# Kernel tuning notes

Measured on AMD Instinct MI355X. Metric: run time of the kernel, lower is better.

The kernel has to match this reference:

```python
import jax, jax.numpy as jnp
import numpy as np


def setup_inputs() -> dict:
    key = jax.random.key(0)
    k1, k2, k3, k4 = jax.random.split(key, 4)
    B, H, S, D = 2, 16, 2048, 64
    q = jax.random.normal(k1, (B, H, S, D), dtype=jnp.float32)
    k = jax.random.normal(k2, (B, H, S, D), dtype=jnp.float32)
    v = jax.random.normal(k3, (B, H, S, D), dtype=jnp.float32)
    mask = jax.random.randint(k4, (1, 1, S, S), 0, 2, dtype=jnp.int32)
    return {"q": q, "k": k, "v": v, "mask": mask}


def reference(q, k, v, mask):
    # scores: [B,H,S,S] -- intentionally materialized as in the original
    d = k.shape[-1]
    scale = 1.0 / jnp.sqrt(jnp.asarray(d, dtype=q.dtype))
    x = jnp.einsum("bhqd,bhkd->bhqk", q, k) * scale
    x = x + mask.astype(x.dtype) * jnp.asarray(-10000.0, dtype=x.dtype)
    p = jax.nn.softmax(x, axis=-1)  # dropout is identity in eval mode
    return jnp.einsum("bhqk,bhkd->bhqd", p, v)
```

## Files before the change

### kernel.cpp

```cpp
#include <hip/hip_runtime.h>


#define S_LEN 2048
#define D_DIM 64
#define N_KT 32
#define LDK 72
#define LDV 72
#define TILE_SHORTS (64 * 72)
#define TILE_BYTES (TILE_SHORTS * 2)
#define NBH 32

typedef __attribute__((ext_vector_type(8))) short bf16x8;
typedef __attribute__((ext_vector_type(16))) float f32x16;
typedef __attribute__((ext_vector_type(2))) __fp16 fp16x2;
typedef unsigned int u32;
typedef unsigned long long u64;

#define C1 0.180336880111121f
#define CM (-14426.9504088896f)

static __device__ __forceinline__ unsigned short f2bf(float f) {
  union { float f; unsigned u; } x; x.f = f;
  return (unsigned short)((x.u + 0x8000u) >> 16);
}
static __device__ __forceinline__ unsigned packbf(float lo, float hi) {
  union { float f; unsigned u; } a, b; a.f = lo; b.f = hi;
  return ((a.u + 0x8000u) >> 16) | ((b.u + 0x8000u) & 0xffff0000u);
}
static __device__ __forceinline__ f32x16 zero16() {
  f32x16 z;
#pragma unroll
  for (int i = 0; i < 16; ++i) z[i] = 0.f;
  return z;
}
static __device__ __forceinline__ void dma16(const u32* g, u32* l) {
  __builtin_amdgcn_global_load_lds(
      (const __attribute__((address_space(1))) u32*)g,
      (__attribute__((address_space(3))) u32*)l, 16, 0, 0);
}
static __device__ __forceinline__ unsigned pkh(float lo, float hi) {
  union { fp16x2 h; unsigned u; } x;
  x.h = __builtin_amdgcn_cvt_pkrtz(lo, hi);
  return x.u;
}

__global__ __launch_bounds__(256) void prep_kv(
    const float* __restrict__ k, const float* __restrict__ v,
    unsigned short* __restrict__ kws, unsigned short* __restrict__ vws) {
  const int kt = blockIdx.x, bh = blockIdx.y;
  const int t = threadIdx.x;
  __shared__ unsigned short Vt[TILE_SHORTS];
  const size_t goff = (size_t)bh * (S_LEN * D_DIM) + (size_t)kt * 64 * D_DIM;
  const float4* kg = (const float4*)(k + goff);
  const float4* vg = (const float4*)(v + goff);
  unsigned short* kimg = kws + (size_t)(bh * N_KT + kt) * TILE_SHORTS;
#pragma unroll
  for (int j = 0; j < 4; ++j) {
    const int i = t + j * 256;
    const int row = i >> 4, c4 = i & 15;
    const float4 x = kg[i];
    ushort4 w;
    w.x = f2bf(x.x); w.y = f2bf(x.y); w.z = f2bf(x.z); w.w = f2bf(x.w);
    *(ushort4*)&kimg[row * LDK + c4 * 4] = w;
    const float4 y = vg[i];
    const int swc = 8 * (((row >> 3) + c4) & 7) + (row & 7);
    const unsigned p01 = pkh(y.x, y.y);
    const unsigned p23 = pkh(y.z, y.w);
    Vt[(4 * c4 + 0) * LDV + swc] = (unsigned short)(p01 & 0xffff);
    Vt[(4 * c4 + 1) * LDV + swc] = (unsigned short)(p01 >> 16);
    Vt[(4 * c4 + 2) * LDV + swc] = (unsigned short)(p23 & 0xffff);
    Vt[(4 * c4 + 3) * LDV + swc] = (unsigned short)(p23 >> 16);
  }
  __syncthreads();
  uint4* vimg = (uint4*)(vws + (size_t)(bh * N_KT + kt) * TILE_SHORTS);
  const uint4* lv = (const uint4*)Vt;
  for (int i = t; i < TILE_BYTES / 16; i += 256) vimg[i] = lv[i];
}

__global__ __launch_bounds__(256) void prep_mask(
    const int* __restrict__ mask, u32* __restrict__ mw) {
  const int wid = blockIdx.x * 4 + (threadIdx.x >> 6);
  const int lane = threadIdx.x & 63;
  const int row = wid >> 5, kt = wid & 31;
  const int mv = mask[(size_t)row * S_LEN + kt * 64 + lane];
  const u64 b = __ballot(mv != 0);
  if (lane < 32) {
    const int hl = lane >> 4, p = lane & 15;
    const int kb = p >> 3, g = (p >> 1) & 3, h = p & 1;
    const int j0 = 32 * kb + 8 * g + 4 * hl + 2 * h;
    u32 w = 0;
    if (!((b >> j0) & 1)) w |= 0x0000FFFFu;
    if (!((b >> (j0 + 1)) & 1)) w |= 0xFFFF0000u;
    mw[((size_t)(row * 2 + hl) * N_KT + kt) * 16 + p] = w;
  }
}

__global__ __launch_bounds__(128, 2) void attn_fwd(
    const float* __restrict__ q, const unsigned short* __restrict__ kws,
    const unsigned short* __restrict__ vws, const u32* __restrict__ mw,
    float* __restrict__ out) {
  const int qt = blockIdx.x;
  const int bh = blockIdx.y;
  const size_t hoff = (size_t)bh * (S_LEN * D_DIM);

  __shared__ unsigned short Ks[2][TILE_SHORTS];
  __shared__ unsigned short Vt[2][TILE_SHORTS];

  const int t = threadIdx.x;
  const int wave = t >> 6;
  const int lane = t & 63;
  const int col = lane & 31;
  const int hl = lane >> 5;
  const int sw = col >> 2;

  const int qg = qt * 64 + wave * 32 + col;

  bf16x8 bQ[4];
  {
    const float* qrow = q + hoff + (size_t)qg * D_DIM;
#pragma unroll
    for (int ks = 0; ks < 4; ++ks) {
      const float4 x0 = *(const float4*)(qrow + ks * 16 + hl * 8);
      const float4 x1 = *(const float4*)(qrow + ks * 16 + hl * 8 + 4);
      union { bf16x8 v; unsigned d[4]; } u;
      u.d[0] = packbf(x0.x * C1, x0.y * C1);
      u.d[1] = packbf(x0.z * C1, x0.w * C1);
      u.d[2] = packbf(x1.x * C1, x1.y * C1);
      u.d[3] = packbf(x1.z * C1, x1.w * C1);
      bQ[ks] = u.v;
    }
  }

  bf16x8 onesA;
  {
    union { bf16x8 v; unsigned d[4]; } u;
    u.d[0] = u.d[1] = u.d[2] = u.d[3] = 0x3C003C00u;
    onesA = u.v;
  }

  const unsigned short* kbase = kws + (size_t)bh * N_KT * TILE_SHORTS;
  const unsigned short* vbase = vws + (size_t)bh * N_KT * TILE_SHORTS;

  f32x16 oT0 = zero16(), oT1 = zero16(), oL = zero16();
  const uint4* mrow = (const uint4*)(mw + (size_t)(qg * 2 + hl) * N_KT * 16);

  {
    const u32* g = (const u32*)((wave == 0 ? kbase : vbase));
    u32* l = wave == 0 ? (u32*)&Ks[0][0] : (u32*)&Vt[0][0];
#pragma unroll
    for (int i = 0; i < 9; ++i) dma16(g + i * 256 + lane * 4, l + i * 256);
  }

  for (int kt = 0; kt < N_KT; ++kt) {
    __syncthreads();
    if (kt + 1 < N_KT) {
      const u32* g = (const u32*)((wave == 0 ? kbase : vbase) +
                                  (size_t)(kt + 1) * TILE_SHORTS);
      u32* l = wave == 0 ? (u32*)&Ks[(kt + 1) & 1][0]
                         : (u32*)&Vt[(kt + 1) & 1][0];
#pragma unroll
      for (int i = 0; i < 9; ++i) dma16(g + i * 256 + lane * 4, l + i * 256);
    }
    uint4 mq0 = mrow[kt * 4 + 0], mq1 = mrow[kt * 4 + 1];
    uint4 mq2 = mrow[kt * 4 + 2], mq3 = mrow[kt * 4 + 3];
    const u32 mwv[16] = {mq0.x, mq0.y, mq0.z, mq0.w, mq1.x, mq1.y, mq1.z, mq1.w,
                         mq2.x, mq2.y, mq2.z, mq2.w, mq3.x, mq3.y, mq3.z, mq3.w};
    const unsigned short* Ksb = Ks[kt & 1];
    const unsigned short* Vtb = Vt[kt & 1];

    f32x16 sT0 = zero16(), sT1 = zero16();
#pragma unroll
    for (int ks = 0; ks < 4; ++ks) {
      const bf16x8 aK0 = *(const bf16x8*)&Ksb[col * LDK + ks * 16 + hl * 8];
      const bf16x8 aK1 = *(const bf16x8*)&Ksb[(32 + col) * LDK + ks * 16 + hl * 8];
      sT0 = __builtin_amdgcn_mfma_f32_32x32x16_bf16(aK0, bQ[ks], sT0, 0, 0, 0);
      sT1 = __builtin_amdgcn_mfma_f32_32x32x16_bf16(aK1, bQ[ks], sT1, 0, 0, 0);
    }

    unsigned pw[16];
#pragma unroll
    for (int kb = 0; kb < 2; ++kb) {
      const f32x16 sT = kb ? sT1 : sT0;
#pragma unroll
      for (int g = 0; g < 4; ++g) {
        const float e0 = __builtin_amdgcn_exp2f(sT[g * 4 + 0]);
        const float e1 = __builtin_amdgcn_exp2f(sT[g * 4 + 1]);
        const float e2 = __builtin_amdgcn_exp2f(sT[g * 4 + 2]);
        const float e3 = __builtin_amdgcn_exp2f(sT[g * 4 + 3]);
        pw[kb * 8 + g * 2 + 0] = pkh(e0, e1) & mwv[kb * 8 + g * 2 + 0];
        pw[kb * 8 + g * 2 + 1] = pkh(e2, e3) & mwv[kb * 8 + g * 2 + 1];
      }
    }

#pragma unroll
    for (int ks = 0; ks < 4; ++ks) {
      const int kb = ks >> 1, h = ks & 1;
      const unsigned d0 = pw[kb * 8 + 4 * h + 0], d1 = pw[kb * 8 + 4 * h + 1];
      const unsigned d2 = pw[kb * 8 + 4 * h + 2], d3 = pw[kb * 8 + 4 * h + 3];
      const unsigned s0 = hl ? d0 : d2;
      const unsigned s1 = hl ? d1 : d3;
      const unsigned r0 = (unsigned)__shfl_xor((int)s0, 32);
      const unsigned r1 = (unsigned)__shfl_xor((int)s1, 32);
      union { bf16x8 v; unsigned d[4]; } pf;
      pf.d[0] = hl ? r0 : d0;
      pf.d[1] = hl ? r1 : d1;
      pf.d[2] = hl ? d2 : r0;
      pf.d[3] = hl ? d3 : r1;
      const int cpr = 8 * (((2 * ks + hl) + sw) & 7);
      const bf16x8 aV0 = *(const bf16x8*)&Vtb[col * LDV + cpr];
      const bf16x8 aV1 = *(const bf16x8*)&Vtb[(32 + col) * LDV + cpr];
      oT0 = __builtin_amdgcn_mfma_f32_32x32x16_f16(aV0, pf.v, oT0, 0, 0, 0);
      oT1 = __builtin_amdgcn_mfma_f32_32x32x16_f16(aV1, pf.v, oT1, 0, 0, 0);
      oL = __builtin_amdgcn_mfma_f32_32x32x16_f16(onesA, pf.v, oL, 0, 0, 0);
    }
  }

  const float inv = 1.0f / oL[0];
  float* orow = out + hoff + (size_t)qg * D_DIM;
#pragma unroll
  for (int rg = 0; rg < 4; ++rg) {
    float4 w0, w1;
    w0.x = oT0[rg * 4 + 0] * inv; w0.y = oT0[rg * 4 + 1] * inv;
    w0.z = oT0[rg * 4 + 2] * inv; w0.w = oT0[rg * 4 + 3] * inv;
    w1.x = oT1[rg * 4 + 0] * inv; w1.y = oT1[rg * 4 + 1] * inv;
    w1.z = oT1[rg * 4 + 2] * inv; w1.w = oT1[rg * 4 + 3] * inv;
    *(float4*)(orow + 8 * rg + 4 * hl) = w0;
    *(float4*)(orow + 32 + 8 * rg + 4 * hl) = w1;
  }
}

__global__ __launch_bounds__(256, 2) void attn_fwd_self(
    const float* __restrict__ q, const float* __restrict__ k,
    const float* __restrict__ v, const int* __restrict__ mask,
    float* __restrict__ out) {
  const int qt = blockIdx.x;
  const int bh = blockIdx.y;
  const size_t hoff = (size_t)bh * (S_LEN * D_DIM);
  __shared__ unsigned short Ks[64 * LDK];
  __shared__ unsigned short Vt[64 * LDV];
  const int t = threadIdx.x;
  const int wave = t >> 6;
  const int lane = t & 63;
  const int col = lane & 31;
  const int hl = lane >> 5;
  const int sw = col >> 2;
  const int qg = qt * 128 + wave * 32 + col;
  bf16x8 bQ[4];
  {
    const float* qrow = q + hoff + (size_t)qg * D_DIM;
#pragma unroll
    for (int ks = 0; ks < 4; ++ks) {
      const float4 x0 = *(const float4*)(qrow + ks * 16 + hl * 8);
      const float4 x1 = *(const float4*)(qrow + ks * 16 + hl * 8 + 4);
      union { bf16x8 v; unsigned d[4]; } u;
      u.d[0] = packbf(x0.x, x0.y);
      u.d[1] = packbf(x0.z, x0.w);
      u.d[2] = packbf(x1.x, x1.y);
      u.d[3] = packbf(x1.z, x1.w);
      bQ[ks] = u.v;
    }
  }
  float4 pk[4], pv[4];
  {
    const float4* kg = (const float4*)(k + hoff);
    const float4* vg = (const float4*)(v + hoff);
#pragma unroll
    for (int j = 0; j < 4; ++j) { pk[j] = kg[t + j * 256]; pv[j] = vg[t + j * 256]; }
  }
  f32x16 oT0 = zero16(), oT1 = zero16();
  float lacc = 0.f;
  const int* mrow = mask + (size_t)qg * S_LEN;
  for (int kt = 0; kt < N_KT; ++kt) {
    __syncthreads();
#pragma unroll
    for (int j = 0; j < 4; ++j) {
      const int i = t + j * 256;
      const int row = i >> 4, c4 = i & 15;
      ushort4 w;
      w.x = f2bf(pk[j].x); w.y = f2bf(pk[j].y);
      w.z = f2bf(pk[j].z); w.w = f2bf(pk[j].w);
      *(ushort4*)&Ks[row * LDK + c4 * 4] = w;
      const int swc = 8 * (((row >> 3) + c4) & 7) + (row & 7);
      Vt[(4 * c4 + 0) * LDV + swc] = f2bf(pv[j].x);
      Vt[(4 * c4 + 1) * LDV + swc] = f2bf(pv[j].y);
      Vt[(4 * c4 + 2) * LDV + swc] = f2bf(pv[j].z);
      Vt[(4 * c4 + 3) * LDV + swc] = f2bf(pv[j].w);
    }
    __syncthreads();
    if (kt + 1 < N_KT) {
      const float4* kg = (const float4*)(k + hoff + (size_t)(kt + 1) * 64 * D_DIM);
      const float4* vg = (const float4*)(v + hoff + (size_t)(kt + 1) * 64 * D_DIM);
#pragma unroll
      for (int j = 0; j < 4; ++j) { pk[j] = kg[t + j * 256]; pv[j] = vg[t + j * 256]; }
    }
    int4 mq[2][4];
#pragma unroll
    for (int kb = 0; kb < 2; ++kb)
#pragma unroll
      for (int g = 0; g < 4; ++g)
        mq[kb][g] = *(const int4*)(mrow + kt * 64 + kb * 32 + g * 8 + hl * 4);
    f32x16 sT0 = zero16(), sT1 = zero16();
#pragma unroll
    for (int ks = 0; ks < 4; ++ks) {
      const bf16x8 aK0 = *(const bf16x8*)&Ks[col * LDK + ks * 16 + hl * 8];
      const bf16x8 aK1 = *(const bf16x8*)&Ks[(32 + col) * LDK + ks * 16 + hl * 8];
      sT0 = __builtin_amdgcn_mfma_f32_32x32x16_bf16(aK0, bQ[ks], sT0, 0, 0, 0);
      sT1 = __builtin_amdgcn_mfma_f32_32x32x16_bf16(aK1, bQ[ks], sT1, 0, 0, 0);
    }
    unsigned pw[2][8];
#pragma unroll
    for (int kb = 0; kb < 2; ++kb) {
      const f32x16 sT = kb ? sT1 : sT0;
      float e[16];
#pragma unroll
      for (int g = 0; g < 4; ++g) {
        const int4 mv = mq[kb][g];
        const int* mvp = &mv.x;
#pragma unroll
        for (int r3 = 0; r3 < 4; ++r3) {
          const int reg = g * 4 + r3;
          const float bias = mvp[r3] ? CM : 0.0f;
          const float ev = __builtin_amdgcn_exp2f(fmaf(sT[reg], C1, bias));
          e[reg] = ev;
          lacc += ev;
        }
        pw[kb][g * 2 + 0] = packbf(e[g * 4 + 0], e[g * 4 + 1]);
        pw[kb][g * 2 + 1] = packbf(e[g * 4 + 2], e[g * 4 + 3]);
      }
    }
#pragma unroll
    for (int ks = 0; ks < 4; ++ks) {
      const int kb = ks >> 1, h = ks & 1;
      const unsigned d0 = pw[kb][4 * h + 0], d1 = pw[kb][4 * h + 1];
      const unsigned d2 = pw[kb][4 * h + 2], d3 = pw[kb][4 * h + 3];
      const unsigned s0 = hl ? d0 : d2;
      const unsigned s1 = hl ? d1 : d3;
      const unsigned r0 = (unsigned)__shfl_xor((int)s0, 32);
      const unsigned r1 = (unsigned)__shfl_xor((int)s1, 32);
      union { bf16x8 v; unsigned d[4]; } pf;
      pf.d[0] = hl ? r0 : d0;
      pf.d[1] = hl ? r1 : d1;
      pf.d[2] = hl ? d2 : r0;
      pf.d[3] = hl ? d3 : r1;
      const int cpr = 8 * (((2 * ks + hl) + sw) & 7);
      const bf16x8 aV0 = *(const bf16x8*)&Vt[col * LDV + cpr];
      const bf16x8 aV1 = *(const bf16x8*)&Vt[(32 + col) * LDV + cpr];
      oT0 = __builtin_amdgcn_mfma_f32_32x32x16_bf16(aV0, pf.v, oT0, 0, 0, 0);
      oT1 = __builtin_amdgcn_mfma_f32_32x32x16_bf16(aV1, pf.v, oT1, 0, 0, 0);
    }
  }
  const float ltot = lacc + __shfl_xor(lacc, 32);
  const float inv = 1.0f / ltot;
  float* orow = out + hoff + (size_t)qg * D_DIM;
#pragma unroll
  for (int rg = 0; rg < 4; ++rg) {
    float4 w0, w1;
    w0.x = oT0[rg * 4 + 0] * inv; w0.y = oT0[rg * 4 + 1] * inv;
    w0.z = oT0[rg * 4 + 2] * inv; w0.w = oT0[rg * 4 + 3] * inv;
    w1.x = oT1[rg * 4 + 0] * inv; w1.y = oT1[rg * 4 + 1] * inv;
    w1.z = oT1[rg * 4 + 2] * inv; w1.w = oT1[rg * 4 + 3] * inv;
    *(float4*)(orow + 8 * rg + 4 * hl) = w0;
    *(float4*)(orow + 32 + 8 * rg + 4 * hl) = w1;
  }
}

extern "C" void kernel_launch(void* const* d_in, const int* in_sizes, int n_in,
                              void* d_out, int out_size, void* d_ws, size_t ws_size,
                              hipStream_t stream) {
  const float* q = (const float*)d_in[0];
  const float* k = (const float*)d_in[1];
  const float* v = (const float*)d_in[2];
  const int* mask = (const int*)d_in[3];
  float* out = (float*)d_out;

  const size_t img_elems = (size_t)NBH * N_KT * TILE_SHORTS;
  const size_t mw_words = (size_t)S_LEN * 2 * N_KT * 16;
  const size_t need = img_elems * 2 * sizeof(unsigned short) + mw_words * 4;

  if (ws_size >= need) {
    unsigned short* kws = (unsigned short*)d_ws;
    unsigned short* vws = kws + img_elems;
    u32* mwp = (u32*)(vws + img_elems);
    prep_kv<<<dim3(N_KT, NBH), dim3(256), 0, stream>>>(k, v, kws, vws);
    prep_mask<<<dim3((S_LEN * N_KT) / 4), dim3(256), 0, stream>>>(mask, mwp);
    attn_fwd<<<dim3(S_LEN / 64, NBH), dim3(128), 0, stream>>>(q, kws, vws, mwp, out);
  } else {
    attn_fwd_self<<<dim3(S_LEN / 128, NBH), dim3(256), 0, stream>>>(q, k, v, mask, out);
  }
}
```

Measured before the change: 169.8 us.

## Load K/V MFMA fragments directly from global into registers, drop LDS staging

The prep kernel now writes K and V in a pre-swizzled per-lane MFMA fragment layout, so the attention kernel can load each operand fragment straight from global memory into registers instead of DMA-ing tiles into LDS. K for the next tile is prefetched into registers, and the LDS double buffers and per-iteration __syncthreads are removed. The mask workspace is reordered kt-major so loads across lanes are more contiguous. In exchange, register pressure rises (K current/next plus V fragments), and each wave re-reads K/V from L2 rather than sharing them through LDS, which could expose global latency.

```diff
diff --git a/kernel.cpp b/kernel.cpp
--- a/kernel.cpp
+++ b/kernel.cpp
@@ -4,11 +4,8 @@
 #define S_LEN 2048
 #define D_DIM 64
 #define N_KT 32
-#define LDK 72
-#define LDV 72
-#define TILE_SHORTS (64 * 72)
-#define TILE_BYTES (TILE_SHORTS * 2)
 #define NBH 32
+#define TILE_FR 4096
 
 typedef __attribute__((ext_vector_type(8))) short bf16x8;
 typedef __attribute__((ext_vector_type(16))) float f32x16;
@@ -18,6 +15,8 @@
 
 #define C1 0.180336880111121f
 #define CM (-14426.9504088896f)
+#define LDK 72
+#define LDV 72
 
 static __device__ __forceinline__ unsigned short f2bf(float f) {
   union { float f; unsigned u; } x; x.f = f;
@@ -32,49 +31,52 @@
 #pragma unroll
   for (int i = 0; i < 16; ++i) z[i] = 0.f;
   return z;
-}
-static __device__ __forceinline__ void dma16(const u32* g, u32* l) {
-  __builtin_amdgcn_global_load_lds(
-      (const __attribute__((address_space(1))) u32*)g,
-      (__attribute__((address_space(3))) u32*)l, 16, 0, 0);
 }
 static __device__ __forceinline__ unsigned pkh(float lo, float hi) {
   union { fp16x2 h; unsigned u; } x;
   x.h = __builtin_amdgcn_cvt_pkrtz(lo, hi);
   return x.u;
 }
-
-__global__ __launch_bounds__(256) void prep_kv(
+static __device__ __forceinline__ unsigned short f2h(float f) {
+  union { fp16x2 h; unsigned u; } x;
+  x.h = __builtin_amdgcn_cvt_pkrtz(f, f);
+  return (unsigned short)x.u;
+}
+
+__global__ __launch_bounds__(256) void prep_kvf(
     const float* __restrict__ k, const float* __restrict__ v,
-    unsigned short* __restrict__ kws, unsigned short* __restrict__ vws) {
+    unsigned short* __restrict__ kfw, unsigned short* __restrict__ vfw) {
   const int kt = blockIdx.x, bh = blockIdx.y;
   const int t = threadIdx.x;
-  __shared__ unsigned short Vt[TILE_SHORTS];
   const size_t goff = (size_t)bh * (S_LEN * D_DIM) + (size_t)kt * 64 * D_DIM;
   const float4* kg = (const float4*)(k + goff);
   const float4* vg = (const float4*)(v + goff);
-  unsigned short* kimg = kws + (size_t)(bh * N_KT + kt) * TILE_SHORTS;
+  unsigned short* kimg = kfw + (size_t)(bh * N_KT + kt) * TILE_FR;
+  unsigned short* vimg = vfw + (size_t)(bh * N_KT + kt) * TILE_FR;
 #pragma unroll
   for (int j = 0; j < 4; ++j) {
     const int i = t + j * 256;
     const int row = i >> 4, c4 = i & 15;
-    const float4 x = kg[i];
-    ushort4 w;
-    w.x = f2bf(x.x); w.y = f2bf(x.y); w.z = f2bf(x.z); w.w = f2bf(x.w);
-    *(ushort4*)&kimg[row * LDK + c4 * 4] = w;
-    const float4 y = vg[i];
-    const int swc = 8 * (((row >> 3) + c4) & 7) + (row & 7);
-    const unsigned p01 = pkh(y.x, y.y);
-    const unsigned p23 = pkh(y.z, y.w);
-    Vt[(4 * c4 + 0) * LDV + swc] = (unsigned short)(p01 & 0xffff);
-    Vt[(4 * c4 + 1) * LDV + swc] = (unsigned short)(p01 >> 16);
-    Vt[(4 * c4 + 2) * LDV + swc] = (unsigned short)(p23 & 0xffff);
-    Vt[(4 * c4 + 3) * LDV + swc] = (unsigned short)(p23 >> 16);
-  }
-  __syncthreads();
-  uint4* vimg = (uint4*)(vws + (size_t)(bh * N_KT + kt) * TILE_SHORTS);
-  const uint4* lv = (const uint4*)Vt;
-  for (int i = t; i < TILE_BYTES / 16; i += 256) vimg[i] = lv[i];
+    {
+      const float4 x = kg[i];
+      const int frag = row >> 5, colr = row & 31;
+      const int ks = c4 >> 2, hlk = (c4 >> 1) & 1, half = c4 & 1;
+      ushort4 w;
+      w.x = f2bf(x.x); w.y = f2bf(x.y); w.z = f2bf(x.z); w.w = f2bf(x.w);
+      *(ushort4*)&kimg[((ks * 2 + frag) * 64 + hlk * 32 + colr) * 8 + half * 4] = w;
+    }
+    {
+      const float4 y = vg[i];
+      const int ksv = row >> 4, hlv = (row >> 3) & 1, pos = row & 7;
+      const float* yp = &y.x;
+#pragma unroll
+      for (int e = 0; e < 4; ++e) {
+        const int d = c4 * 4 + e;
+        vimg[((ksv * 2 + (d >> 5)) * 64 + hlv * 32 + (d & 31)) * 8 + pos] =
+            f2h(yp[e]);
+      }
+    }
+  }
 }
 
 __global__ __launch_bounds__(256) void prep_mask(
@@ -91,27 +93,23 @@
     u32 w = 0;
     if (!((b >> j0) & 1)) w |= 0x0000FFFFu;
     if (!((b >> (j0 + 1)) & 1)) w |= 0xFFFF0000u;
-    mw[((size_t)(row * 2 + hl) * N_KT + kt) * 16 + p] = w;
+    mw[(((size_t)kt * S_LEN + row) * 2 + hl) * 16 + p] = w;
   }
 }
 
 __global__ __launch_bounds__(128, 2) void attn_fwd(
-    const float* __restrict__ q, const unsigned short* __restrict__ kws,
-    const unsigned short* __restrict__ vws, const u32* __restrict__ mw,
+    const float* __restrict__ q, const unsigned short* __restrict__ kf,
+    const unsigned short* __restrict__ vf, const u32* __restrict__ mw,
     float* __restrict__ out) {
   const int qt = blockIdx.x;
   const int bh = blockIdx.y;
   const size_t hoff = (size_t)bh * (S_LEN * D_DIM);
-
-  __shared__ unsigned short Ks[2][TILE_SHORTS];
-  __shared__ unsigned short Vt[2][TILE_SHORTS];
 
   const int t = threadIdx.x;
   const int wave = t >> 6;
   const int lane = t & 63;
   const int col = lane & 31;
   const int hl = lane >> 5;
-  const int sw = col >> 2;
 
   const int qg = qt * 64 + wave * 32 + col;
 
@@ -138,45 +136,39 @@
     onesA = u.v;
   }
 
-  const unsigned short* kbase = kws + (size_t)bh * N_KT * TILE_SHORTS;
-  const unsigned short* vbase = vws + (size_t)bh * N_KT * TILE_SHORTS;
+  const unsigned short* kbase =
+      kf + (size_t)bh * N_KT * TILE_FR + (size_t)lane * 8;
+  const unsigned short* vbase =
+      vf + (size_t)bh * N_KT * TILE_FR + (size_t)lane * 8;
+  const uint4* mrow = (const uint4*)mw + ((size_t)qg * 2 + hl) * 4;
 
   f32x16 oT0 = zero16(), oT1 = zero16(), oL = zero16();
-  const uint4* mrow = (const uint4*)(mw + (size_t)(qg * 2 + hl) * N_KT * 16);
-
-  {
-    const u32* g = (const u32*)((wave == 0 ? kbase : vbase));
-    u32* l = wave == 0 ? (u32*)&Ks[0][0] : (u32*)&Vt[0][0];
-#pragma unroll
-    for (int i = 0; i < 9; ++i) dma16(g + i * 256 + lane * 4, l + i * 256);
-  }
+
+  bf16x8 kc[8], kn[8], vc[8];
+#pragma unroll
+  for (int i = 0; i < 8; ++i) kc[i] = *(const bf16x8*)(kbase + i * 512);
 
   for (int kt = 0; kt < N_KT; ++kt) {
-    __syncthreads();
+    const unsigned short* vt = vbase + (size_t)kt * TILE_FR;
+#pragma unroll
+    for (int i = 0; i < 8; ++i) vc[i] = *(const bf16x8*)(vt + i * 512);
+    const uint4* mt = mrow + (size_t)kt * (S_LEN * 2 * 4);
+    const uint4 m0 = mt[0], m1 = mt[1], m2 = mt[2], m3 = mt[3];
     if (kt + 1 < N_KT) {
-      const u32* g = (const u32*)((wave == 0 ? kbase : vbase) +
-                                  (size_t)(kt + 1) * TILE_SHORTS);
-      u32* l = wave == 0 ? (u32*)&Ks[(kt + 1) & 1][0]
-                         : (u32*)&Vt[(kt + 1) & 1][0];
-#pragma unroll
-      for (int i = 0; i < 9; ++i) dma16(g + i * 256 + lane * 4, l + i * 256);
-    }
-    uint4 mq0 = mrow[kt * 4 + 0], mq1 = mrow[kt * 4 + 1];
-    uint4 mq2 = mrow[kt * 4 + 2], mq3 = mrow[kt * 4 + 3];
-    const u32 mwv[16] = {mq0.x, mq0.y, mq0.z, mq0.w, mq1.x, mq1.y, mq1.z, mq1.w,
-                         mq2.x, mq2.y, mq2.z, mq2.w, mq3.x, mq3.y, mq3.z, mq3.w};
-    const unsigned short* Ksb = Ks[kt & 1];
-    const unsigned short* Vtb = Vt[kt & 1];
+      const unsigned short* nt = kbase + (size_t)(kt + 1) * TILE_FR;
+#pragma unroll
+      for (int i = 0; i < 8; ++i) kn[i] = *(const bf16x8*)(nt + i * 512);
+    }
 
     f32x16 sT0 = zero16(), sT1 = zero16();
 #pragma unroll
     for (int ks = 0; ks < 4; ++ks) {
-      const bf16x8 aK0 = *(const bf16x8*)&Ksb[col * LDK + ks * 16 + hl * 8];
-      const bf16x8 aK1 = *(const bf16x8*)&Ksb[(32 + col) * LDK + ks * 16 + hl * 8];
-      sT0 = __builtin_amdgcn_mfma_f32_32x32x16_bf16(aK0, bQ[ks], sT0, 0, 0, 0);
-      sT1 = __builtin_amdgcn_mfma_f32_32x32x16_bf16(aK1, bQ[ks], sT1, 0, 0, 0);
-    }
-
+      sT0 = __builtin_amdgcn_mfma_f32_32x32x16_bf16(kc[ks * 2 + 0], bQ[ks], sT0, 0, 0, 0);
+      sT1 = __builtin_amdgcn_mfma_f32_32x32x16_bf16(kc[ks * 2 + 1], bQ[ks], sT1, 0, 0, 0);
+    }
+
+    const u32 mwv[16] = {m0.x, m0.y, m0.z, m0.w, m1.x, m1.y, m1.z, m1.w,
+                         m2.x, m2.y, m2.z, m2.w, m3.x, m3.y, m3.z, m3.w};
     unsigned pw[16];
 #pragma unroll
     for (int kb = 0; kb < 2; ++kb) {
@@ -206,13 +198,13 @@
       pf.d[1] = hl ? r1 : d1;
       pf.d[2] = hl ? d2 : r0;
       pf.d[3] = hl ? d3 : r1;
-      const int cpr = 8 * (((2 * ks + hl) + sw) & 7);
-      const bf16x8 aV0 = *(const bf16x8*)&Vtb[col * LDV + cpr];
-      const bf16x8 aV1 = *(const bf16x8*)&Vtb[(32 + col) * LDV + cpr];
-      oT0 = __builtin_amdgcn_mfma_f32_32x32x16_f16(aV0, pf.v, oT0, 0, 0, 0);
-      oT1 = __builtin_amdgcn_mfma_f32_32x32x16_f16(aV1, pf.v, oT1, 0, 0, 0);
+      oT0 = __builtin_amdgcn_mfma_f32_32x32x16_f16(vc[ks * 2 + 0], pf.v, oT0, 0, 0, 0);
+      oT1 = __builtin_amdgcn_mfma_f32_32x32x16_f16(vc[ks * 2 + 1], pf.v, oT1, 0, 0, 0);
       oL = __builtin_amdgcn_mfma_f32_32x32x16_f16(onesA, pf.v, oL, 0, 0, 0);
     }
+
+#pragma unroll
+    for (int i = 0; i < 8; ++i) kc[i] = kn[i];
   }
 
   const float inv = 1.0f / oL[0];
@@ -373,17 +365,17 @@
   const int* mask = (const int*)d_in[3];
   float* out = (float*)d_out;
 
-  const size_t img_elems = (size_t)NBH * N_KT * TILE_SHORTS;
-  const size_t mw_words = (size_t)S_LEN * 2 * N_KT * 16;
+  const size_t img_elems = (size_t)NBH * N_KT * TILE_FR;
+  const size_t mw_words = (size_t)N_KT * S_LEN * 2 * 16;
   const size_t need = img_elems * 2 * sizeof(unsigned short) + mw_words * 4;
 
   if (ws_size >= need) {
-    unsigned short* kws = (unsigned short*)d_ws;
-    unsigned short* vws = kws + img_elems;
-    u32* mwp = (u32*)(vws + img_elems);
-    prep_kv<<<dim3(N_KT, NBH), dim3(256), 0, stream>>>(k, v, kws, vws);
+    unsigned short* kfw = (unsigned short*)d_ws;
+    unsigned short* vfw = kfw + img_elems;
+    u32* mwp = (u32*)(vfw + img_elems);
+    prep_kvf<<<dim3(N_KT, NBH), dim3(256), 0, stream>>>(k, v, kfw, vfw);
     prep_mask<<<dim3((S_LEN * N_KT) / 4), dim3(256), 0, stream>>>(mask, mwp);
-    attn_fwd<<<dim3(S_LEN / 64, NBH), dim3(128), 0, stream>>>(q, kws, vws, mwp, out);
+    attn_fwd<<<dim3(S_LEN / 64, NBH), dim3(128), 0, stream>>>(q, kfw, vfw, mwp, out);
   } else {
     attn_fwd_self<<<dim3(S_LEN / 128, NBH), dim3(256), 0, stream>>>(q, k, v, mask, out);
   }
```

New measurement: 181.8 us. 7.0% more time.
